# Kernel tuning notes

Hardware: AMD Instinct MI355X
Metric: run time of the kernel (lower is better)

Reference implementation:

```python
import jax, jax.numpy as jnp
import numpy as np

N = 100000      # total nodes in batched graph
E = 3200000     # total edges (avg degree 32)
G = 128         # number of graphs in batch
F_IN = 512      # raw node feature dim
NC = 128        # num_classes = projected feature dim (GraphConv layer-0 input)
HID = 256       # hid_channels
OUT = 10        # out_channels
LYR = 3         # args.lyr
EPS = 1e-5      # BatchNorm1d eps


def setup_inputs() -> dict:
    key = jax.random.key(0)
    ks = jax.random.split(key, 20)
    h = jax.random.normal(ks[0], (N, F_IN), dtype=jnp.float32)
    src = jax.random.randint(ks[1], (E,), 0, N, dtype=jnp.int32)
    dst = jax.random.randint(ks[2], (E,), 0, N, dtype=jnp.int32)
    # contiguous sorted graph assignment: every graph non-empty
    graph_ids = (jnp.arange(N, dtype=jnp.int32) * G) // N
    w_init = jax.random.normal(ks[3], (NC, F_IN), dtype=jnp.float32) * 0.05
    inp = dict(h=h, src=src, dst=dst, graph_ids=graph_ids, w_init=w_init)
    dims = [NC, HID, HID]
    for i in range(LYR):
        inp[f"lw{i}"] = jax.random.normal(ks[4 + i], (dims[i], HID), dtype=jnp.float32) * 0.05
        inp[f"lb{i}"] = jnp.zeros((HID,), jnp.float32)
        inp[f"gamma{i}"] = jnp.ones((HID,), jnp.float32)
        inp[f"beta{i}"] = jnp.zeros((HID,), jnp.float32)
    inp["fc_w"] = jax.random.normal(ks[10], (HID, OUT), dtype=jnp.float32) * 0.05
    inp["fc_b"] = jnp.zeros((OUT,), jnp.float32)
    return inp


def _forward(h, src, dst, graph_ids, w_init, layers, fc_w, fc_b):
    # symmetric normalization (DGL GraphConv norm='both')
    ones_e = jnp.ones((E,), h.dtype)
    out_deg = jax.ops.segment_sum(ones_e, src, num_segments=N)
    in_deg = jax.ops.segment_sum(ones_e, dst, num_segments=N)
    norm_src = jnp.where(out_deg > 0, out_deg ** -0.5, 0.0)  # [N]
    norm_dst = jnp.where(in_deg > 0, in_deg ** -0.5, 0.0)    # [N]

    h = h @ w_init.T  # [N, NC]
    for (lw, lb, gamma, beta) in layers:
        # GraphConv: (D_out^-1/2) gather -> scatter-sum -> (D_in^-1/2), then linear
        m = (h * norm_src[:, None])[src]                       # [E, d]
        agg = jax.ops.segment_sum(m, dst, num_segments=N)       # [N, d]
        h = (agg * norm_dst[:, None]) @ lw + lb                 # [N, HID]
        # BatchNorm1d (training-mode batch stats, biased variance) + ReLU
        mu = jnp.mean(h, axis=0)
        var = jnp.mean((h - mu) ** 2, axis=0)
        h = jax.nn.relu((h - mu) * jax.lax.rsqrt(var + EPS) * gamma + beta)
    # dgl.max_nodes: per-graph max over nodes
    hg = jax.ops.segment_max(h, graph_ids, num_segments=G)      # [G, HID]
    return hg @ fc_w + fc_b                                     # [G, OUT]


def reference(h, src, dst, graph_ids, w_init,
              lw0, lb0, gamma0, beta0,
              lw1, lb1, gamma1, beta1,
              lw2, lb2, gamma2, beta2,
              fc_w, fc_b):
    layers = [(lw0, lb0, gamma0, beta0),
              (lw1, lb1, gamma1, beta1),
              (lw2, lb2, gamma2, beta2)]
    return _forward(h, src, dst, graph_ids, w_init, layers, fc_w, fc_b)
```

## Files before the change

kernel.cpp:

```cpp
#include <hip/hip_runtime.h>
#include <hip/hip_bf16.h>

#define N_NODES 100000
#define N_EDGES 3200000
#define N_GRAPHS 128
#define FIN 512
#define NCLS 128
#define HID 256
#define OUT_DIM 10
#define BN_EPS 1e-5f

#define NBUCK 391
#define EPB   ((N_EDGES + NBUCK - 1) / NBUCK)
#define STATS_CPY 1536

typedef unsigned short ush;
typedef ush su16x8 __attribute__((ext_vector_type(8)));
typedef ush su16x4 __attribute__((ext_vector_type(4)));
typedef __bf16 bf16x8v __attribute__((ext_vector_type(8)));
typedef float f32x4v __attribute__((ext_vector_type(4)));

__device__ __forceinline__ float bf2f(ush u) {
    union { unsigned int i; float f; } v; v.i = ((unsigned int)u) << 16; return v.f;
}
__device__ __forceinline__ ush f2bf(float f) {
    __hip_bfloat16 b = __float2bfloat16(f);
    return __builtin_bit_cast(ush, b);
}

template <typename T>
__device__ __forceinline__ auto mfma_sel(T a, T b, f32x4v c, int)
    -> decltype(__builtin_amdgcn_mfma_f32_16x16x32_bf16(a, b, c, 0, 0, 0)) {
    return __builtin_amdgcn_mfma_f32_16x16x32_bf16(a, b, c, 0, 0, 0);
}
template <typename T>
__device__ __forceinline__ f32x4v mfma_sel(T a, T b, f32x4v c, long) {
    return __builtin_amdgcn_mfma_f32_16x16x32_bf16(
        __builtin_bit_cast(bf16x8v, a), __builtin_bit_cast(bf16x8v, b), c, 0, 0, 0);
}
__device__ __forceinline__ f32x4v MFMA_BF16(su16x8 a, su16x8 b, f32x4v c) {
    return mfma_sel(a, b, c, 0);
}

__global__ void zero_kernel(int* __restrict__ odeg8, int* __restrict__ bcnt,
                            float* __restrict__ stats8, float* __restrict__ hg) {
    int i = blockIdx.x * 256 + threadIdx.x;
    if (i < 8 * N_NODES) odeg8[i] = 0;
    if (i <= NBUCK) bcnt[i] = 0;
    if (i < 8 * STATS_CPY) stats8[i] = 0.f;
    if (i < N_GRAPHS * HID) hg[i] = 0.f;
}

__global__ __launch_bounds__(256) void edge_pass1(const int* __restrict__ src,
                                                  const int* __restrict__ dst,
                                                  int* __restrict__ odeg8,
                                                  int* __restrict__ hist,
                                                  int* __restrict__ bcnt) {
    __shared__ int hc[NBUCK];
    int tid = threadIdx.x, blk = blockIdx.x;
    for (int i = tid; i < NBUCK; i += 256) hc[i] = 0;
    __syncthreads();
    int e0 = blk * EPB, e1 = e0 + EPB; if (e1 > N_EDGES) e1 = N_EDGES;
    int c = blk & 7;
    for (int e = e0 + tid; e < e1; e += 256) {
        atomicAdd(&odeg8[(size_t)c * N_NODES + src[e]], 1);
        atomicAdd(&hc[dst[e] >> 8], 1);
    }
    __syncthreads();
    for (int i = tid; i < NBUCK; i += 256) {
        int v = hc[i];
        hist[(size_t)blk * NBUCK + i] = v;
        if (v) atomicAdd(&bcnt[i], v);
    }
}

#define CVT_TOTAL (NCLS * FIN + HID * NCLS + HID * HID + HID * HID)
__global__ void misc_prep(const int* __restrict__ odeg8, float* __restrict__ nsrc,
                          const int* __restrict__ gids, int* __restrict__ gstart,
                          const float* __restrict__ w0, const float* __restrict__ l0,
                          const float* __restrict__ l1, const float* __restrict__ l2,
                          ush* __restrict__ wB0, ush* __restrict__ t0,
                          ush* __restrict__ t1, ush* __restrict__ t2) {
    int i = blockIdx.x * 256 + threadIdx.x;
    if (i < N_NODES) {
        int od = 0;
        #pragma unroll
        for (int c = 0; c < 8; c++) od += odeg8[(size_t)c * N_NODES + i];
        nsrc[i] = od > 0 ? rsqrtf((float)od) : 0.f;
        int g = gids[i];
        int gp = (i == 0) ? -1 : gids[i - 1];
        for (int gg = gp + 1; gg <= g; gg++) gstart[gg] = i;
        if (i == N_NODES - 1) {
            for (int gg = g + 1; gg <= N_GRAPHS; gg++) gstart[gg] = N_NODES;
        }
        return;
    }
    i -= N_NODES;
    if (i < NCLS * FIN) { wB0[i] = f2bf(w0[i]); return; }
    i -= NCLS * FIN;
    if (i < HID * NCLS) { int n = i >> 7, k = i & 127; t0[i] = f2bf(l0[k * HID + n]); return; }
    i -= HID * NCLS;
    if (i < HID * HID) { int n = i >> 8, k = i & 255; t1[i] = f2bf(l1[k * HID + n]); return; }
    i -= HID * HID;
    if (i < HID * HID) { int n = i >> 8, k = i & 255; t2[i] = f2bf(l2[k * HID + n]); }
}

__global__ __launch_bounds__(512) void bscan_kernel(const int* __restrict__ bcnt,
                                                    int* __restrict__ bbase) {
    __shared__ int a[512];
    int tid = threadIdx.x;
    int v = (tid < NBUCK) ? bcnt[tid] : 0;
    a[tid] = v;
    __syncthreads();
    for (int s = 1; s < 512; s <<= 1) {
        int y = (tid >= s) ? a[tid - s] : 0;
        __syncthreads();
        a[tid] += y;
        __syncthreads();
    }
    if (tid < NBUCK) bbase[tid] = a[tid] - v;
    if (tid == 0) bbase[NBUCK] = N_EDGES;
}

__global__ __launch_bounds__(512) void boff_kernel(const int* __restrict__ hist,
                                                   const int* __restrict__ bbase,
                                                   int* __restrict__ off) {
    __shared__ int a[512];
    int b = blockIdx.x, tid = threadIdx.x;
    int v = (tid < NBUCK) ? hist[(size_t)tid * NBUCK + b] : 0;
    a[tid] = v;
    __syncthreads();
    for (int s = 1; s < 512; s <<= 1) {
        int y = (tid >= s) ? a[tid - s] : 0;
        __syncthreads();
        a[tid] += y;
        __syncthreads();
    }
    if (tid < NBUCK) off[(size_t)tid * NBUCK + b] = bbase[b] + a[tid] - v;
}

__global__ __launch_bounds__(256) void stage_kernel(const int* __restrict__ src,
                                                    const int* __restrict__ dst,
                                                    const int* __restrict__ off,
                                                    unsigned int* __restrict__ staged) {
    __shared__ int cur[NBUCK];
    int tid = threadIdx.x, blk = blockIdx.x;
    for (int i = tid; i < NBUCK; i += 256) cur[i] = off[(size_t)blk * NBUCK + i];
    __syncthreads();
    int e0 = blk * EPB, e1 = e0 + EPB; if (e1 > N_EDGES) e1 = N_EDGES;
    for (int e = e0 + tid; e < e1; e += 256) {
        int d = dst[e], s = src[e];
        int pos = atomicAdd(&cur[d >> 8], 1);
        staged[pos] = ((unsigned int)(d & 255) << 24) | (unsigned int)s;
    }
}

__global__ __launch_bounds__(256) void csr_kernel(const unsigned int* __restrict__ staged,
                                                  const int* __restrict__ bbase,
                                                  int* __restrict__ roff,
                                                  float* __restrict__ ndst,
                                                  int* __restrict__ csr) {
    __shared__ int cnt[256], pfx[256], cur[256];
    int b = blockIdx.x, tid = threadIdx.x;
    int beg = bbase[b], end = bbase[b + 1];
    int nodeBase = b * 256;
    int nNodes = N_NODES - nodeBase; if (nNodes > 256) nNodes = 256;
    cnt[tid] = 0;
    __syncthreads();
    for (int e = beg + tid; e < end; e += 256) atomicAdd(&cnt[staged[e] >> 24], 1);
    __syncthreads();
    int v = cnt[tid];
    pfx[tid] = v;
    __syncthreads();
    for (int s = 1; s < 256; s <<= 1) {
        int y = (tid >= s) ? pfx[tid - s] : 0;
        __syncthreads();
        pfx[tid] += y;
        __syncthreads();
    }
    int excl = pfx[tid] - v;
    pfx[tid] = excl;
    cur[tid] = 0;
    if (tid < nNodes) {
        int node = nodeBase + tid;
        roff[node] = beg + excl;
        ndst[node] = v > 0 ? rsqrtf((float)v) : 0.f;
    }
    if (b == NBUCK - 1 && tid == 0) roff[N_NODES] = N_EDGES;
    __syncthreads();
    for (int e = beg + tid; e < end; e += 256) {
        unsigned int w = staged[e];
        int dl = w >> 24;
        int pos = beg + pfx[dl] + atomicAdd(&cur[dl], 1);
        csr[pos] = (int)(w & 0xFFFFFFu);
    }
}

template <bool A_F32, bool DO_STATS>
__global__ __launch_bounds__(256) void mfma_gemm(
    const void* __restrict__ Aptr, const ush* __restrict__ BT,
    ush* __restrict__ C, int M, int K, int NN,
    const float* __restrict__ rowscale, const float* __restrict__ bias,
    float* __restrict__ stats)
{
    __shared__ __align__(16) ush As[128][40];
    __shared__ __align__(16) ush Bs[128][40];
    const int bn0 = blockIdx.x * 128;
    const int bm0 = blockIdx.y * 128;
    const int tid = threadIdx.x;
    const int lane = tid & 63;
    const int wv = tid >> 6;
    const int wm = (wv >> 1) * 64;
    const int wn = (wv & 1) * 64;
    const int lm = lane & 15;
    const int lg = lane >> 4;

    f32x4v zero = {0.f, 0.f, 0.f, 0.f};
    f32x4v acc[4][4];
    #pragma unroll
    for (int mi = 0; mi < 4; mi++)
        #pragma unroll
        for (int ni = 0; ni < 4; ni++) acc[mi][ni] = zero;

    for (int k0 = 0; k0 < K; k0 += 32) {
        #pragma unroll
        for (int i = 0; i < 2; i++) {
            int seg = tid + i * 256;
            int n = seg >> 2, kp = seg & 3;
            su16x8 v = *(const su16x8*)&BT[(size_t)(bn0 + n) * K + k0 + kp * 8];
            *(su16x8*)&Bs[n][kp * 8] = v;
        }
        if constexpr (A_F32) {
            const float* Af = (const float*)Aptr;
            #pragma unroll
            for (int i = 0; i < 4; i++) {
                int seg = tid + i * 256;
                int m = seg >> 3, kp = seg & 7;
                int gm = bm0 + m; if (gm >= M) gm = M - 1;
                float4 v = *(const float4*)&Af[(size_t)gm * K + k0 + kp * 4];
                su16x4 o = { f2bf(v.x), f2bf(v.y), f2bf(v.z), f2bf(v.w) };
                *(su16x4*)&As[m][kp * 4] = o;
            }
        } else {
            const ush* Ab = (const ush*)Aptr;
            #pragma unroll
            for (int i = 0; i < 2; i++) {
                int seg = tid + i * 256;
                int m = seg >> 2, kp = seg & 3;
                int gm = bm0 + m; if (gm >= M) gm = M - 1;
                su16x8 v = *(const su16x8*)&Ab[(size_t)gm * K + k0 + kp * 8];
                *(su16x8*)&As[m][kp * 8] = v;
            }
        }
        __syncthreads();
        su16x8 af[4], bfr[4];
        #pragma unroll
        for (int i = 0; i < 4; i++)
            af[i] = *(const su16x8*)&As[wm + i * 16 + lm][lg * 8];
        #pragma unroll
        for (int i = 0; i < 4; i++)
            bfr[i] = *(const su16x8*)&Bs[wn + i * 16 + lm][lg * 8];
        #pragma unroll
        for (int mi = 0; mi < 4; mi++)
            #pragma unroll
            for (int ni = 0; ni < 4; ni++)
                acc[mi][ni] = MFMA_BF16(af[mi], bfr[ni], acc[mi][ni]);
        __syncthreads();
    }

    float s4[4] = {0.f, 0.f, 0.f, 0.f}, q4[4] = {0.f, 0.f, 0.f, 0.f};
    #pragma unroll
    for (int mi = 0; mi < 4; mi++) {
        #pragma unroll
        for (int j = 0; j < 4; j++) {
            int gm = bm0 + wm + mi * 16 + lg * 4 + j;
            bool valid = gm < M;
            float rs = (rowscale && valid) ? rowscale[gm] : 1.f;
            #pragma unroll
            for (int ni = 0; ni < 4; ni++) {
                int gn = bn0 + wn + ni * 16 + lm;
                float v = acc[mi][ni][j] * rs;
                if (bias) v += bias[gn];
                if (valid) {
                    C[(size_t)gm * NN + gn] = f2bf(v);
                    if constexpr (DO_STATS) { s4[ni] += v; q4[ni] += v * v; }
                }
            }
        }
    }
    if constexpr (DO_STATS) {
        float* st = stats + ((blockIdx.x + gridDim.x * blockIdx.y) & 7) * STATS_CPY;
        #pragma unroll
        for (int ni = 0; ni < 4; ni++) {
            s4[ni] += __shfl_xor(s4[ni], 16); s4[ni] += __shfl_xor(s4[ni], 32);
            q4[ni] += __shfl_xor(q4[ni], 16); q4[ni] += __shfl_xor(q4[ni], 32);
        }
        if (lg == 0) {
            #pragma unroll
            for (int ni = 0; ni < 4; ni++) {
                int gn = bn0 + wn + ni * 16 + lm;
                atomicAdd(&st[gn], s4[ni]);
                atomicAdd(&st[HID + gn], q4[ni]);
            }
        }
    }
}

__global__ __launch_bounds__(256) void agg128(const ush* __restrict__ hs,
                                              const int* __restrict__ roff,
                                              const int* __restrict__ csr,
                                              ush* __restrict__ out)
{
    int node = (blockIdx.x * 256 + threadIdx.x) >> 6;
    int lane = threadIdx.x & 63;
    if (node >= N_NODES) return;
    int q = lane >> 4;
    int c0 = (lane & 15) * 8;
    int beg = roff[node], end = roff[node + 1];
    int len = end - beg;
    int s = beg + ((len * q) >> 2);
    int t = beg + ((len * (q + 1)) >> 2);
    float a0[8] = {}, a1[8] = {}, a2[8] = {}, a3[8] = {};
    int e = s;
    for (; e + 3 < t; e += 4) {
        int i0 = csr[e], i1 = csr[e + 1], i2 = csr[e + 2], i3 = csr[e + 3];
        su16x8 v0 = *(const su16x8*)&hs[(size_t)i0 * 128 + c0];
        su16x8 v1 = *(const su16x8*)&hs[(size_t)i1 * 128 + c0];
        su16x8 v2 = *(const su16x8*)&hs[(size_t)i2 * 128 + c0];
        su16x8 v3 = *(const su16x8*)&hs[(size_t)i3 * 128 + c0];
        #pragma unroll
        for (int j = 0; j < 8; j++) {
            a0[j] += bf2f(v0[j]); a1[j] += bf2f(v1[j]);
            a2[j] += bf2f(v2[j]); a3[j] += bf2f(v3[j]);
        }
    }
    for (; e < t; e++) {
        int i0 = csr[e];
        su16x8 v0 = *(const su16x8*)&hs[(size_t)i0 * 128 + c0];
        #pragma unroll
        for (int j = 0; j < 8; j++) a0[j] += bf2f(v0[j]);
    }
    #pragma unroll
    for (int j = 0; j < 8; j++) {
        a0[j] += a1[j] + a2[j] + a3[j];
        a0[j] += __shfl_xor(a0[j], 16);
        a0[j] += __shfl_xor(a0[j], 32);
    }
    if (lane < 16) {
        su16x8 o;
        #pragma unroll
        for (int j = 0; j < 8; j++) o[j] = f2bf(a0[j]);
        __builtin_nontemporal_store(o, (su16x8*)&out[(size_t)node * 128 + c0]);
    }
}

__global__ __launch_bounds__(256) void agg256(const ush* __restrict__ Q,
                                              const int* __restrict__ roff,
                                              const int* __restrict__ csr,
                                              ush* __restrict__ out)
{
    int node = (blockIdx.x * 256 + threadIdx.x) >> 6;
    int lane = threadIdx.x & 63;
    if (node >= N_NODES) return;
    int half = lane >> 5;
    int c0 = (lane & 31) * 8;
    int beg = roff[node], end = roff[node + 1];
    int len = end - beg;
    int s = beg + ((len * half) >> 1);
    int t = beg + ((len * (half + 1)) >> 1);
    float a0[8] = {}, a1[8] = {}, a2[8] = {}, a3[8] = {};
    int e = s;
    for (; e + 3 < t; e += 4) {
        int i0 = csr[e], i1 = csr[e + 1], i2 = csr[e + 2], i3 = csr[e + 3];
        su16x8 v0 = *(const su16x8*)&Q[(size_t)i0 * 256 + c0];
        su16x8 v1 = *(const su16x8*)&Q[(size_t)i1 * 256 + c0];
        su16x8 v2 = *(const su16x8*)&Q[(size_t)i2 * 256 + c0];
        su16x8 v3 = *(const su16x8*)&Q[(size_t)i3 * 256 + c0];
        #pragma unroll
        for (int j = 0; j < 8; j++) {
            a0[j] += bf2f(v0[j]); a1[j] += bf2f(v1[j]);
            a2[j] += bf2f(v2[j]); a3[j] += bf2f(v3[j]);
        }
    }
    for (; e < t; e++) {
        int i0 = csr[e];
        su16x8 v0 = *(const su16x8*)&Q[(size_t)i0 * 256 + c0];
        #pragma unroll
        for (int j = 0; j < 8; j++) a0[j] += bf2f(v0[j]);
    }
    #pragma unroll
    for (int j = 0; j < 8; j++) {
        a0[j] += a1[j] + a2[j] + a3[j];
        a0[j] += __shfl_xor(a0[j], 32);
    }
    if (lane < 32) {
        su16x8 o;
        #pragma unroll
        for (int j = 0; j < 8; j++) o[j] = f2bf(a0[j]);
        __builtin_nontemporal_store(o, (su16x8*)&out[(size_t)node * 256 + c0]);
    }
}

__global__ __launch_bounds__(256) void bnq_kernel(const ush* __restrict__ P,
                                                  const float* __restrict__ stats,
                                                  const float* __restrict__ gamma,
                                                  const float* __restrict__ beta,
                                                  const float* __restrict__ nsrc,
                                                  ush* __restrict__ Q)
{
    __shared__ float sa[HID], sb[HID];
    int tid = threadIdx.x;
    {
        float ssum = 0.f, qsum = 0.f;
        #pragma unroll
        for (int c8 = 0; c8 < 8; c8++) {
            ssum += stats[c8 * STATS_CPY + tid];
            qsum += stats[c8 * STATS_CPY + HID + tid];
        }
        const float inv_n = 1.f / (float)N_NODES;
        float mu = ssum * inv_n;
        float var = fmaf(-mu, mu, qsum * inv_n);
        float a = gamma[tid] * rsqrtf(var + BN_EPS);
        sa[tid] = a;
        sb[tid] = fmaf(-mu, a, beta[tid]);
    }
    __syncthreads();
    const int total = N_NODES * 32;
    for (int idx = blockIdx.x * 256 + tid; idx < total; idx += gridDim.x * 256) {
        int r = idx >> 5, c0 = (idx & 31) * 8;
        su16x8 v = __builtin_nontemporal_load((const su16x8*)&P[(size_t)r * HID + c0]);
        float ns = nsrc[r];
        su16x8 o;
        #pragma unroll
        for (int j = 0; j < 8; j++) {
            float x = fmaxf(fmaf(bf2f(v[j]), sa[c0 + j], sb[c0 + j]), 0.f) * ns;
            o[j] = f2bf(x);
        }
        *(su16x8*)&Q[(size_t)r * HID + c0] = o;
    }
}

__global__ __launch_bounds__(256) void segmax_ab(const ush* __restrict__ pre,
                                                 const float* __restrict__ stats,
                                                 const float* __restrict__ gamma,
                                                 const float* __restrict__ beta,
                                                 const int* __restrict__ gstart,
                                                 float* __restrict__ hg) {
    int c = threadIdx.x;
    float ssum = 0.f, qsum = 0.f;
    #pragma unroll
    for (int c8 = 0; c8 < 8; c8++) {
        ssum += stats[c8 * STATS_CPY + c];
        qsum += stats[c8 * STATS_CPY + HID + c];
    }
    const float inv_n = 1.f / (float)N_NODES;
    float mu = ssum * inv_n;
    float var = fmaf(-mu, mu, qsum * inv_n);
    float a = gamma[c] * rsqrtf(var + BN_EPS);
    float b = fmaf(-mu, a, beta[c]);
    int g = blockIdx.x;
    int chunk = blockIdx.y;
    int beg = gstart[g], end = gstart[g + 1];
    int len = end - beg;
    int per = (len + 7) >> 3;
    int s = beg + chunk * per;
    int e = s + per; if (e > end) e = end;
    float m0 = 0.f, m1 = 0.f;
    int n = s;
    for (; n + 1 < e; n += 2) {
        m0 = fmaxf(m0, fmaf(bf2f(pre[(size_t)n * HID + c]), a, b));
        m1 = fmaxf(m1, fmaf(bf2f(pre[(size_t)(n + 1) * HID + c]), a, b));
    }
    if (n < e) m0 = fmaxf(m0, fmaf(bf2f(pre[(size_t)n * HID + c]), a, b));
    float m = fmaxf(fmaxf(m0, m1), 0.f);
    atomicMax((int*)&hg[g * HID + c], __float_as_int(m));
}

__global__ void fc_kernel(const float* __restrict__ hg, const float* __restrict__ w,
                          const float* __restrict__ b, float* __restrict__ out) {
    int idx = blockIdx.x * 256 + threadIdx.x;
    if (idx >= N_GRAPHS * OUT_DIM) return;
    int g = idx / OUT_DIM, j = idx % OUT_DIM;
    float s = b[j];
    for (int c = 0; c < HID; c++) s += hg[g * HID + c] * w[c * OUT_DIM + j];
    out[idx] = s;
}

extern "C" void kernel_launch(void* const* d_in, const int* in_sizes, int n_in,
                              void* d_out, int out_size, void* d_ws, size_t ws_size,
                              hipStream_t stream) {
    const float* h      = (const float*)d_in[0];
    const int*   src    = (const int*)d_in[1];
    const int*   dst    = (const int*)d_in[2];
    const int*   gids   = (const int*)d_in[3];
    const float* w_init = (const float*)d_in[4];
    const float* lw[3]    = { (const float*)d_in[5],  (const float*)d_in[9],  (const float*)d_in[13] };
    const float* lb[3]    = { (const float*)d_in[6],  (const float*)d_in[10], (const float*)d_in[14] };
    const float* gamma[3] = { (const float*)d_in[7],  (const float*)d_in[11], (const float*)d_in[15] };
    const float* beta[3]  = { (const float*)d_in[8],  (const float*)d_in[12], (const float*)d_in[16] };
    const float* fc_w = (const float*)d_in[17];
    const float* fc_b = (const float*)d_in[18];
    float* out = (float*)d_out;

    char* ws = (char*)d_ws;
    size_t off_b = 0;
    auto alloc = [&](size_t bytes) { size_t o = off_b; off_b += (bytes + 255) & ~(size_t)255; return o; };
    size_t o_h0s   = alloc((size_t)N_NODES * NCLS * 2);
    size_t o_aggb  = alloc((size_t)N_NODES * HID * 2);
    size_t o_P     = alloc((size_t)N_NODES * HID * 2);
    size_t o_Q     = alloc((size_t)N_NODES * HID * 2);
    size_t o_wB0   = alloc((size_t)NCLS * FIN * 2);
    size_t o_lwT0  = alloc((size_t)HID * NCLS * 2);
    size_t o_lwT1  = alloc((size_t)HID * HID * 2);
    size_t o_lwT2  = alloc((size_t)HID * HID * 2);
    size_t o_nsrc  = alloc((size_t)N_NODES * 4);
    size_t o_ndst  = alloc((size_t)N_NODES * 4);
    size_t o_odeg8 = alloc((size_t)8 * N_NODES * 4);
    size_t o_roff  = alloc((size_t)(N_NODES + 1) * 4);
    size_t o_csr   = alloc((size_t)N_EDGES * 4);
    size_t o_stg   = alloc((size_t)N_EDGES * 4);
    size_t o_hist  = alloc((size_t)NBUCK * NBUCK * 4);
    size_t o_off   = alloc((size_t)NBUCK * NBUCK * 4);
    size_t o_bcnt  = alloc((size_t)(NBUCK + 1) * 4);
    size_t o_bbase = alloc((size_t)(NBUCK + 1) * 4);
    size_t o_stat8 = alloc((size_t)8 * STATS_CPY * 4);
    size_t o_gst   = alloc((size_t)(N_GRAPHS + 1) * 4);
    size_t o_hg    = alloc((size_t)N_GRAPHS * HID * 4);
    if (off_b > ws_size) return;

    ush*   h0s  = (ush*)(ws + o_h0s);
    ush*   aggb = (ush*)(ws + o_aggb);
    ush*   P    = (ush*)(ws + o_P);
    ush*   Q    = (ush*)(ws + o_Q);
    ush*   wB0  = (ush*)(ws + o_wB0);
    ush*   lwT[3] = { (ush*)(ws + o_lwT0), (ush*)(ws + o_lwT1), (ush*)(ws + o_lwT2) };
    float* nsrc = (float*)(ws + o_nsrc);
    float* ndst = (float*)(ws + o_ndst);
    int*   odeg8= (int*)(ws + o_odeg8);
    int*   roff = (int*)(ws + o_roff);
    int*   csr  = (int*)(ws + o_csr);
    unsigned int* stg = (unsigned int*)(ws + o_stg);
    int*   hist = (int*)(ws + o_hist);
    int*   boff = (int*)(ws + o_off);
    int*   bcnt = (int*)(ws + o_bcnt);
    int*   bbase= (int*)(ws + o_bbase);
    float* stats8 = (float*)(ws + o_stat8);
    int*   gst  = (int*)(ws + o_gst);
    float* hg   = (float*)(ws + o_hg);

    zero_kernel<<<(8 * N_NODES + 255) / 256, 256, 0, stream>>>(odeg8, bcnt, stats8, hg);

    edge_pass1<<<NBUCK, 256, 0, stream>>>(src, dst, odeg8, hist, bcnt);

    misc_prep<<<(N_NODES + CVT_TOTAL + 255) / 256, 256, 0, stream>>>(
        odeg8, nsrc, gids, gst, w_init, lw[0], lw[1], lw[2], wB0, lwT[0], lwT[1], lwT[2]);

    bscan_kernel<<<1, 512, 0, stream>>>(bcnt, bbase);
    boff_kernel<<<NBUCK, 512, 0, stream>>>(hist, bbase, boff);
    stage_kernel<<<NBUCK, 256, 0, stream>>>(src, dst, boff, stg);
    csr_kernel<<<NBUCK, 256, 0, stream>>>(stg, bbase, roff, ndst, csr);

    const int mblocks = (N_NODES + 127) / 128;
    const int aggblocks = (N_NODES * 64 + 255) / 256;

    {
        dim3 grid(NCLS / 128, mblocks);
        mfma_gemm<true, false><<<grid, 256, 0, stream>>>(h, wB0, h0s, N_NODES, FIN, NCLS,
                                                         nsrc, nullptr, nullptr);
    }

    agg128<<<aggblocks, 256, 0, stream>>>(h0s, roff, csr, aggb);
    {
        dim3 grid(HID / 128, mblocks);
        mfma_gemm<false, true><<<grid, 256, 0, stream>>>(aggb, lwT[0], P, N_NODES, NCLS, HID,
                                                         ndst, lb[0], stats8 + 0 * 2 * HID);
    }

    for (int l = 1; l < 3; l++) {
        bnq_kernel<<<1024, 256, 0, stream>>>(P, stats8 + (l - 1) * 2 * HID,
                                             gamma[l - 1], beta[l - 1], nsrc, Q);
        agg256<<<aggblocks, 256, 0, stream>>>(Q, roff, csr, aggb);
        dim3 grid(HID / 128, mblocks);
        mfma_gemm<false, true><<<grid, 256, 0, stream>>>(aggb, lwT[l], P, N_NODES, HID, HID,
                                                         ndst, lb[l], stats8 + l * 2 * HID);
    }

    {
        dim3 grid(N_GRAPHS, 8);
        segmax_ab<<<grid, 256, 0, stream>>>(P, stats8 + 2 * 2 * HID, gamma[2], beta[2], gst, hg);
    }
    fc_kernel<<<(N_GRAPHS * OUT_DIM + 255) / 256, 256, 0, stream>>>(hg, fc_w, fc_b, out);
}
```

Baseline: 1.072 ms.

## Quantize post-BN node features to uint8 with per-row scale for aggregation

```diff
diff --git a/kernel.cpp b/kernel.cpp
--- a/kernel.cpp
+++ b/kernel.cpp
@@ -354,15 +354,17 @@
     }
 }
 
-__global__ __launch_bounds__(256) void agg256(const ush* __restrict__ Q,
-                                              const int* __restrict__ roff,
-                                              const int* __restrict__ csr,
-                                              ush* __restrict__ out)
+__global__ __launch_bounds__(256) void agg256_u8(const unsigned int* __restrict__ Qp,
+                                                 const float* __restrict__ qs,
+                                                 const int* __restrict__ roff,
+                                                 const int* __restrict__ csr,
+                                                 ush* __restrict__ out)
 {
     int node = (blockIdx.x * 256 + threadIdx.x) >> 6;
     int lane = threadIdx.x & 63;
     if (node >= N_NODES) return;
     int half = lane >> 5;
+    int cu = (lane & 31) * 2;
     int c0 = (lane & 31) * 8;
     int beg = roff[node], end = roff[node + 1];
     int len = end - beg;
@@ -372,21 +374,32 @@
     int e = s;
     for (; e + 3 < t; e += 4) {
         int i0 = csr[e], i1 = csr[e + 1], i2 = csr[e + 2], i3 = csr[e + 3];
-        su16x8 v0 = *(const su16x8*)&Q[(size_t)i0 * 256 + c0];
-        su16x8 v1 = *(const su16x8*)&Q[(size_t)i1 * 256 + c0];
-        su16x8 v2 = *(const su16x8*)&Q[(size_t)i2 * 256 + c0];
-        su16x8 v3 = *(const su16x8*)&Q[(size_t)i3 * 256 + c0];
-        #pragma unroll
-        for (int j = 0; j < 8; j++) {
-            a0[j] += bf2f(v0[j]); a1[j] += bf2f(v1[j]);
-            a2[j] += bf2f(v2[j]); a3[j] += bf2f(v3[j]);
+        float s0 = qs[i0], s1 = qs[i1], s2 = qs[i2], s3 = qs[i3];
+        uint2 v0 = *(const uint2*)&Qp[(size_t)i0 * 64 + cu];
+        uint2 v1 = *(const uint2*)&Qp[(size_t)i1 * 64 + cu];
+        uint2 v2 = *(const uint2*)&Qp[(size_t)i2 * 64 + cu];
+        uint2 v3 = *(const uint2*)&Qp[(size_t)i3 * 64 + cu];
+        #pragma unroll
+        for (int j = 0; j < 4; j++) {
+            a0[j]     = fmaf((float)((v0.x >> (8 * j)) & 255u), s0, a0[j]);
+            a0[4 + j] = fmaf((float)((v0.y >> (8 * j)) & 255u), s0, a0[4 + j]);
+            a1[j]     = fmaf((float)((v1.x >> (8 * j)) & 255u), s1, a1[j]);
+            a1[4 + j] = fmaf((float)((v1.y >> (8 * j)) & 255u), s1, a1[4 + j]);
+            a2[j]     = fmaf((float)((v2.x >> (8 * j)) & 255u), s2, a2[j]);
+            a2[4 + j] = fmaf((float)((v2.y >> (8 * j)) & 255u), s2, a2[4 + j]);
+            a3[j]     = fmaf((float)((v3.x >> (8 * j)) & 255u), s3, a3[j]);
+            a3[4 + j] = fmaf((float)((v3.y >> (8 * j)) & 255u), s3, a3[4 + j]);
         }
     }
     for (; e < t; e++) {
         int i0 = csr[e];
-        su16x8 v0 = *(const su16x8*)&Q[(size_t)i0 * 256 + c0];
-        #pragma unroll
-        for (int j = 0; j < 8; j++) a0[j] += bf2f(v0[j]);
+        float s0 = qs[i0];
+        uint2 v0 = *(const uint2*)&Qp[(size_t)i0 * 64 + cu];
+        #pragma unroll
+        for (int j = 0; j < 4; j++) {
+            a0[j]     = fmaf((float)((v0.x >> (8 * j)) & 255u), s0, a0[j]);
+            a0[4 + j] = fmaf((float)((v0.y >> (8 * j)) & 255u), s0, a0[4 + j]);
+        }
     }
     #pragma unroll
     for (int j = 0; j < 8; j++) {
@@ -401,12 +414,13 @@
     }
 }
 
-__global__ __launch_bounds__(256) void bnq_kernel(const ush* __restrict__ P,
-                                                  const float* __restrict__ stats,
-                                                  const float* __restrict__ gamma,
-                                                  const float* __restrict__ beta,
-                                                  const float* __restrict__ nsrc,
-                                                  ush* __restrict__ Q)
+__global__ __launch_bounds__(256) void bnq_u8(const ush* __restrict__ P,
+                                              const float* __restrict__ stats,
+                                              const float* __restrict__ gamma,
+                                              const float* __restrict__ beta,
+                                              const float* __restrict__ nsrc,
+                                              unsigned int* __restrict__ Qp,
+                                              float* __restrict__ qs)
 {
     __shared__ float sa[HID], sb[HID];
     int tid = threadIdx.x;
@@ -425,18 +439,29 @@
         sb[tid] = fmaf(-mu, a, beta[tid]);
     }
     __syncthreads();
-    const int total = N_NODES * 32;
-    for (int idx = blockIdx.x * 256 + tid; idx < total; idx += gridDim.x * 256) {
-        int r = idx >> 5, c0 = (idx & 31) * 8;
-        su16x8 v = __builtin_nontemporal_load((const su16x8*)&P[(size_t)r * HID + c0]);
+    int lane = tid & 63;
+    int c0 = lane * 4;
+    int wid = (blockIdx.x * 256 + tid) >> 6;
+    const int NW = (1024 * 256) >> 6;
+    float ka0 = sa[c0], ka1 = sa[c0 + 1], ka2 = sa[c0 + 2], ka3 = sa[c0 + 3];
+    float kb0 = sb[c0], kb1 = sb[c0 + 1], kb2 = sb[c0 + 2], kb3 = sb[c0 + 3];
+    for (int r = wid; r < N_NODES; r += NW) {
+        su16x4 v = *(const su16x4*)&P[(size_t)r * HID + c0];
         float ns = nsrc[r];
-        su16x8 o;
-        #pragma unroll
-        for (int j = 0; j < 8; j++) {
-            float x = fmaxf(fmaf(bf2f(v[j]), sa[c0 + j], sb[c0 + j]), 0.f) * ns;
-            o[j] = f2bf(x);
-        }
-        *(su16x8*)&Q[(size_t)r * HID + c0] = o;
+        float x0 = fmaxf(fmaf(bf2f(v[0]), ka0, kb0), 0.f) * ns;
+        float x1 = fmaxf(fmaf(bf2f(v[1]), ka1, kb1), 0.f) * ns;
+        float x2 = fmaxf(fmaf(bf2f(v[2]), ka2, kb2), 0.f) * ns;
+        float x3 = fmaxf(fmaf(bf2f(v[3]), ka3, kb3), 0.f) * ns;
+        float m = fmaxf(fmaxf(x0, x1), fmaxf(x2, x3));
+        #pragma unroll
+        for (int off = 1; off < 64; off <<= 1) m = fmaxf(m, __shfl_xor(m, off));
+        float inv = m > 0.f ? 255.0f / m : 0.f;
+        unsigned q0 = (unsigned)fminf(fmaf(x0, inv, 0.5f), 255.f);
+        unsigned q1 = (unsigned)fminf(fmaf(x1, inv, 0.5f), 255.f);
+        unsigned q2 = (unsigned)fminf(fmaf(x2, inv, 0.5f), 255.f);
+        unsigned q3 = (unsigned)fminf(fmaf(x3, inv, 0.5f), 255.f);
+        Qp[(size_t)r * 64 + lane] = q0 | (q1 << 8) | (q2 << 16) | (q3 << 24);
+        if (lane == 0) qs[r] = m * (1.0f / 255.0f);
     }
 }
 
@@ -508,7 +533,8 @@
     size_t o_h0s   = alloc((size_t)N_NODES * NCLS * 2);
     size_t o_aggb  = alloc((size_t)N_NODES * HID * 2);
     size_t o_P     = alloc((size_t)N_NODES * HID * 2);
-    size_t o_Q     = alloc((size_t)N_NODES * HID * 2);
+    size_t o_Qp    = alloc((size_t)N_NODES * 64 * 4);
+    size_t o_qsc   = alloc((size_t)N_NODES * 4);
     size_t o_wB0   = alloc((size_t)NCLS * FIN * 2);
     size_t o_lwT0  = alloc((size_t)HID * NCLS * 2);
     size_t o_lwT1  = alloc((size_t)HID * HID * 2);
@@ -531,7 +557,8 @@
     ush*   h0s  = (ush*)(ws + o_h0s);
     ush*   aggb = (ush*)(ws + o_aggb);
     ush*   P    = (ush*)(ws + o_P);
-    ush*   Q    = (ush*)(ws + o_Q);
+    unsigned int* Qp = (unsigned int*)(ws + o_Qp);
+    float* qsc  = (float*)(ws + o_qsc);
     ush*   wB0  = (ush*)(ws + o_wB0);
     ush*   lwT[3] = { (ush*)(ws + o_lwT0), (ush*)(ws + o_lwT1), (ush*)(ws + o_lwT2) };
     float* nsrc = (float*)(ws + o_nsrc);
@@ -577,9 +604,9 @@
     }
 
     for (int l = 1; l < 3; l++) {
-        bnq_kernel<<<1024, 256, 0, stream>>>(P, stats8 + (l - 1) * 2 * HID,
-                                             gamma[l - 1], beta[l - 1], nsrc, Q);
-        agg256<<<aggblocks, 256, 0, stream>>>(Q, roff, csr, aggb);
+        bnq_u8<<<1024, 256, 0, stream>>>(P, stats8 + (l - 1) * 2 * HID,
+                                         gamma[l - 1], beta[l - 1], nsrc, Qp, qsc);
+        agg256_u8<<<aggblocks, 256, 0, stream>>>(Qp, qsc, roff, csr, aggb);
         dim3 grid(HID / 128, mblocks);
         mfma_gemm<false, true><<<grid, 256, 0, stream>>>(aggb, lwT[l], P, N_NODES, HID, HID,
                                                          ndst, lb[l], stats8 + l * 2 * HID);
```

New measurement: 944.8 us. 1.13x faster.
